# Optimization experiments

Hardware: AMD Instinct MI355X
Metric: run time of the kernel (lower is better)

The kernel has to match this reference:

```python
import jax, jax.numpy as jnp
import numpy as np

B, H, S, DK = 2, 16, 2048, 64


def setup_inputs() -> dict:
    key = jax.random.key(0)
    k1, k2, k3, k4 = jax.random.split(key, 4)
    Q = jax.random.normal(k1, (B, H, S, DK), dtype=jnp.float32)
    K = jax.random.normal(k2, (B, H, S, DK), dtype=jnp.float32)
    V = jax.random.normal(k3, (B, H, S, DK), dtype=jnp.float32)
    attn_mask = jax.random.randint(k4, (B, 1, S, S), 0, 2).astype(jnp.bool_)
    return {"Q": Q, "K": K, "V": V, "attn_mask": attn_mask}


def reference(Q, K, V, attn_mask):
    d_k = Q.shape[-1]
    scale = 1.0 / jnp.sqrt(jnp.asarray(d_k, dtype=Q.dtype))
    # scores: [B,H,S,S]
    scores = jnp.einsum('bhqd,bhkd->bhqk', Q, K) * scale
    scores = jnp.where(attn_mask, jnp.asarray(-1e9, dtype=scores.dtype), scores)
    attn = jax.nn.softmax(scores, axis=-1)
    # dropout in eval mode (identity) for deterministic reference
    return jnp.einsum('bhqk,bhkd->bhqd', attn, V)
```

## Files before the change

kernel.cpp:

```cpp
#include <hip/hip_runtime.h>
#include <hip/hip_bf16.h>

#define Bdim 2
#define Hdim 16
#define Sdim 2048
#define Ddim 64
#define KVBLK 64
#define NT (Sdim / KVBLK)
#define WQ 32
#define NWAVE 4
#define QTILE (WQ * NWAVE)
#define QSCL (0.125f * 1.44269504088896f)
#define SCALE 0.125f
#define BUFE 8192
#define VOFF 4096

typedef __bf16 bf16x8 __attribute__((ext_vector_type(8)));
typedef float  f32x4  __attribute__((ext_vector_type(4)));
typedef float  f32x16 __attribute__((ext_vector_type(16)));
typedef unsigned u32x4 __attribute__((ext_vector_type(4)));

__device__ __forceinline__ void gll16(const __bf16* g, __bf16* l) {
  __builtin_amdgcn_global_load_lds(
      (const __attribute__((address_space(1))) void*)g,
      (__attribute__((address_space(3))) void*)l, 16, 0, 0);
}
__device__ __forceinline__ unsigned cvtpk_raw(float lo, float hi) {
  unsigned r;
  asm("v_cvt_pk_bf16_f32 %0, %1, %2" : "=v"(r) : "v"(lo), "v"(hi));
  return r;
}
template <bool SW>
__device__ __forceinline__ unsigned pko(float a, float b) {
  return SW ? cvtpk_raw(b, a) : cvtpk_raw(a, b);
}
__device__ __forceinline__ unsigned cvtpk(float a, float b, bool sw) {
  const float lo = sw ? b : a;
  const float hi = sw ? a : b;
  return cvtpk_raw(lo, hi);
}
template <bool SW>
__device__ __forceinline__ void packAll(const float (&sv0)[16],
                                        const float (&sv1)[16],
                                        unsigned (&pw)[16]) {
#pragma unroll
  for (int ks = 0; ks < 4; ++ks) {
    const int rb = 8 * (ks & 1);
    if (ks < 2) {
      pw[ks * 4 + 0] = pko<SW>(sv0[rb + 0], sv0[rb + 1]);
      pw[ks * 4 + 1] = pko<SW>(sv0[rb + 2], sv0[rb + 3]);
      pw[ks * 4 + 2] = pko<SW>(sv0[rb + 4], sv0[rb + 5]);
      pw[ks * 4 + 3] = pko<SW>(sv0[rb + 6], sv0[rb + 7]);
    } else {
      pw[ks * 4 + 0] = pko<SW>(sv1[rb + 0], sv1[rb + 1]);
      pw[ks * 4 + 1] = pko<SW>(sv1[rb + 2], sv1[rb + 3]);
      pw[ks * 4 + 2] = pko<SW>(sv1[rb + 4], sv1[rb + 5]);
      pw[ks * 4 + 3] = pko<SW>(sv1[rb + 6], sv1[rb + 7]);
    }
  }
}

__global__ __launch_bounds__(256) void prep_all(
    const void* __restrict__ mask, unsigned long long* __restrict__ packed,
    const float* __restrict__ K, const float* __restrict__ V,
    __bf16* __restrict__ Kb, __bf16* __restrict__ Vt) {
  __shared__ __bf16 tile[64][72];
  const int t = threadIdx.x;

  if (blockIdx.x < 512) {
    const int nwords = Bdim * Sdim * (Sdim / 64);
    const unsigned* m32 = (const unsigned*)mask;
    const unsigned char* m8 = (const unsigned char*)mask;
    int gid = blockIdx.x * 256 + t;
    int lane = gid & 63;
    int wid = gid >> 6;
    const int nwaves = 512 * 256 / 64;
    bool isBytes = __any(m32[lane] > 1u);
    for (int w = wid; w < nwords; w += nwaves) {
      int v = isBytes ? (int)m8[(size_t)w * 64 + lane]
                      : (int)m32[(size_t)w * 64 + lane];
      unsigned long long bal = __ballot(v != 0);
      if (lane == 0) packed[w] = bal;
    }
    return;
  }

  const int idx = blockIdx.x - 512;
  const int bh = idx >> 5, st = idx & 31;
  const int r = t >> 2, c0 = (t & 3) << 4;
  {
    const float* ks = K + ((size_t)bh * Sdim + st * 64 + r) * Ddim + c0;
    bf16x8 o0, o1;
#pragma unroll
    for (int j = 0; j < 8; ++j) o0[j] = (__bf16)ks[j];
#pragma unroll
    for (int j = 0; j < 8; ++j) o1[j] = (__bf16)ks[8 + j];
    __bf16* kd = Kb + ((size_t)bh * Sdim + st * 64 + r) * Ddim + c0;
    *(bf16x8*)kd = o0;
    *(bf16x8*)(kd + 8) = o1;
  }
  {
    const float* vs = V + ((size_t)bh * Sdim + st * 64 + r) * Ddim + c0;
#pragma unroll
    for (int j = 0; j < 16; ++j) tile[r][c0 + j] = (__bf16)vs[j];
  }
  __syncthreads();
  {
    const int d = t >> 2, s0 = (t & 3) << 4;
    __bf16 o[16];
#pragma unroll
    for (int j = 0; j < 16; ++j) o[j] = tile[s0 + j][d];
    __bf16* dst = Vt + ((size_t)bh * Ddim + d) * Sdim + st * 64 + s0;
    *(bf16x8*)dst = *(bf16x8*)&o[0];
    *(bf16x8*)(dst + 8) = *(bf16x8*)&o[8];
  }
}

__global__ __launch_bounds__(256, 2) void attn4(
    const float* __restrict__ Q, const __bf16* __restrict__ Kb,
    const __bf16* __restrict__ Vt,
    const unsigned long long* __restrict__ maskP, float* __restrict__ Out) {
  __shared__ alignas(16) __bf16 sm[3 * BUFE];

  const int tid = threadIdx.x;
  const int lane = tid & 63;
  const int w = tid >> 6;
  const int l31 = lane & 31;
  const int hi = lane >> 5;
  const int rsw = l31 & 7;

  const int bid = blockIdx.x;
  const int bh = bid & 31;
  const int qt = bid >> 5;
  const int b = bh >> 4;
  const int qrow = qt * QTILE + w * WQ + l31;

  const __bf16* Kbase = Kb + (size_t)bh * Sdim * Ddim;
  const __bf16* Vbase = Vt + (size_t)bh * (size_t)Ddim * Sdim;
  const unsigned long long* mp =
      maskP + ((size_t)b * Sdim + qrow) * (Sdim / 64);

  const bool sw = (cvtpk_raw(0.0f, 1.0f) & 0xFFFFu) != 0u;

  bf16x8 qf[4];
  {
    const float* qs = Q + ((size_t)bh * Sdim + qrow) * Ddim;
#pragma unroll
    for (int step = 0; step < 4; ++step) {
      const int d0 = step * 16 + hi * 8;
      float4 a = *(const float4*)(qs + d0);
      float4 c = *(const float4*)(qs + d0 + 4);
      u32x4 f;
      f[0] = cvtpk(a.x * QSCL, a.y * QSCL, sw);
      f[1] = cvtpk(a.z * QSCL, a.w * QSCL, sw);
      f[2] = cvtpk(c.x * QSCL, c.y * QSCL, sw);
      f[3] = cvtpk(c.z * QSCL, c.w * QSCL, sw);
      qf[step] = __builtin_bit_cast(bf16x8, f);
    }
  }

  const int srow = 16 * w + (lane >> 3);
  const int sblk = (lane & 7) ^ ((lane >> 3) & 7);
  const int dstw = w * 1024;

#define STAGE(off_, kt_)                                                        \
  do {                                                                          \
    const __bf16* kp_ = Kbase + ((size_t)(kt_)*KVBLK + srow) * Ddim + sblk * 8; \
    gll16(kp_, &sm[(off_) + dstw]);                                             \
    gll16(kp_ + 8 * Ddim, &sm[(off_) + dstw + 512]);                            \
    const __bf16* vp_ =                                                         \
        Vbase + (size_t)srow * Sdim + (size_t)(kt_)*KVBLK + sblk * 8;           \
    gll16(vp_, &sm[(off_) + VOFF + dstw]);                                      \
    gll16(vp_ + 8 * Sdim, &sm[(off_) + VOFF + dstw + 512]);                     \
  } while (0)

  f32x16 otA = {0,0,0,0,0,0,0,0,0,0,0,0,0,0,0,0};
  f32x16 otB = {0,0,0,0,0,0,0,0,0,0,0,0,0,0,0,0};
  float lrow = 0.f;

  unsigned long long mwCur = mp[0];
  STAGE(0, 0);
  int rdOff = 0, stOff = BUFE;

#pragma unroll 1
  for (int kt = 0; kt < NT; ++kt) {
    const unsigned long long mwNext = mp[kt + 1 < NT ? kt + 1 : NT - 1];
    if (kt + 1 < NT) {
      STAGE(stOff, kt + 1);
      asm volatile("s_waitcnt vmcnt(5)" ::: "memory");
    } else {
      asm volatile("s_waitcnt vmcnt(1)" ::: "memory");
    }
    __builtin_amdgcn_s_barrier();
    __builtin_amdgcn_sched_barrier(0);

    f32x16 st0 = {0,0,0,0,0,0,0,0,0,0,0,0,0,0,0,0};
    f32x16 st1 = {0,0,0,0,0,0,0,0,0,0,0,0,0,0,0,0};
    __builtin_amdgcn_s_setprio(1);
#pragma unroll
    for (int step = 0; step < 4; ++step) {
      bf16x8 kf = *(const bf16x8*)&sm[rdOff + l31 * 64 + (((step * 2 + hi) ^ rsw) << 3)];
      st0 = __builtin_amdgcn_mfma_f32_32x32x16_bf16(kf, qf[step], st0, 0, 0, 0);
    }
#pragma unroll
    for (int step = 0; step < 4; ++step) {
      bf16x8 kf = *(const bf16x8*)&sm[rdOff + (32 + l31) * 64 + (((step * 2 + hi) ^ rsw) << 3)];
      st1 = __builtin_amdgcn_mfma_f32_32x32x16_bf16(kf, qf[step], st1, 0, 0, 0);
    }
    __builtin_amdgcn_s_setprio(0);

    float sv0[16], sv1[16];
    const unsigned w0s = ((unsigned)mwCur) >> (hi * 4);
    const unsigned w1s = ((unsigned)(mwCur >> 32)) >> (hi * 4);
#pragma unroll
    for (int r = 0; r < 16; ++r) {
      const int cr = (r & 3) + 8 * (r >> 2);
      const float e0 = __builtin_amdgcn_exp2f(st0[r]);
      const float e1 = __builtin_amdgcn_exp2f(st1[r]);
      sv0[r] = ((w0s >> cr) & 1u) ? 0.f : e0;
      sv1[r] = ((w1s >> cr) & 1u) ? 0.f : e1;
    }

    float s8[8];
#pragma unroll
    for (int j = 0; j < 8; ++j)
      s8[j] = (sv0[j] + sv0[j + 8]) + (sv1[j] + sv1[j + 8]);
    lrow += ((s8[0] + s8[4]) + (s8[1] + s8[5])) +
            ((s8[2] + s8[6]) + (s8[3] + s8[7]));

    unsigned pw[16];
    if (!sw) packAll<false>(sv0, sv1, pw);
    else     packAll<true>(sv0, sv1, pw);
    bf16x8 pb[4];
#pragma unroll
    for (int ks = 0; ks < 4; ++ks) {
      const unsigned W0 = pw[ks * 4 + 0], W1 = pw[ks * 4 + 1];
      const unsigned X0 = pw[ks * 4 + 2], X1 = pw[ks * 4 + 3];
      const unsigned s1 = hi ? W0 : X0;
      const unsigned s2 = hi ? W1 : X1;
      const unsigned r1 = __shfl_xor(s1, 32, 64);
      const unsigned r2 = __shfl_xor(s2, 32, 64);
      u32x4 wv;
      wv[0] = hi ? r1 : W0;
      wv[1] = hi ? r2 : W1;
      wv[2] = hi ? X0 : r1;
      wv[3] = hi ? X1 : r2;
      pb[ks] = __builtin_bit_cast(bf16x8, wv);
    }

    __builtin_amdgcn_s_setprio(1);
#pragma unroll
    for (int ks = 0; ks < 4; ++ks) {
      bf16x8 vf = *(const bf16x8*)&sm[rdOff + VOFF + l31 * 64 + (((ks * 2 + hi) ^ rsw) << 3)];
      otA = __builtin_amdgcn_mfma_f32_32x32x16_bf16(vf, pb[ks], otA, 0, 0, 0);
    }
#pragma unroll
    for (int ks = 0; ks < 4; ++ks) {
      bf16x8 vf = *(const bf16x8*)&sm[rdOff + VOFF + (32 + l31) * 64 + (((ks * 2 + hi) ^ rsw) << 3)];
      otB = __builtin_amdgcn_mfma_f32_32x32x16_bf16(vf, pb[ks], otB, 0, 0, 0);
    }
    __builtin_amdgcn_s_setprio(0);

    mwCur = mwNext;
    rdOff = stOff;
    stOff = (stOff == 2 * BUFE) ? 0 : stOff + BUFE;
  }
#undef STAGE

  lrow += __shfl_xor(lrow, 32, 64);
  const float inv = 1.f / (lrow + 1e-30f);
  float* orow = Out + ((size_t)bh * Sdim + qrow) * Ddim;
#pragma unroll
  for (int g = 0; g < 4; ++g) {
    const int d0 = 8 * g + 4 * hi;
    float4 va = {otA[4 * g] * inv, otA[4 * g + 1] * inv,
                 otA[4 * g + 2] * inv, otA[4 * g + 3] * inv};
    float4 vb = {otB[4 * g] * inv, otB[4 * g + 1] * inv,
                 otB[4 * g + 2] * inv, otB[4 * g + 3] * inv};
    *(float4*)(orow + d0) = va;
    *(float4*)(orow + 32 + d0) = vb;
  }
}

__global__ __launch_bounds__(256) void attn_fallback(
    const float* __restrict__ Q, const float* __restrict__ K,
    const float* __restrict__ V, const void* __restrict__ maskRaw,
    float* __restrict__ Out) {
  __shared__ alignas(16) __bf16 Kl[KVBLK * Ddim];
  __shared__ alignas(16) __bf16 Vts[Ddim * KVBLK];
  __shared__ alignas(16) __bf16 Pl[4][16 * 64];

  const int tid = threadIdx.x;
  const int lane = tid & 63;
  const int w = tid >> 6;
  const int lhi = lane >> 4;
  const int llo = lane & 15;

  const int qt = blockIdx.x;
  const int bh = blockIdx.y;
  const int b = bh >> 4;
  const int qbase = qt * 64;

  const float* Qp = Q + (size_t)bh * Sdim * Ddim;
  const float* Kp = K + (size_t)bh * Sdim * Ddim;
  const float* Vp = V + (size_t)bh * Sdim * Ddim;

  bool maskBytes = __any(((const unsigned*)maskRaw)[lane] > 1u);

  bf16x8 qf0, qf1;
  {
    const int qr = qbase + w * 16 + llo;
    const float* src = Qp + (size_t)qr * Ddim + lhi * 8;
#pragma unroll
    for (int i = 0; i < 8; ++i) qf0[i] = (__bf16)(src[i] * SCALE);
#pragma unroll
    for (int i = 0; i < 8; ++i) qf1[i] = (__bf16)(src[32 + i] * SCALE);
  }

  f32x4 acc[4] = {{0.f,0.f,0.f,0.f},{0.f,0.f,0.f,0.f},
                  {0.f,0.f,0.f,0.f},{0.f,0.f,0.f,0.f}};
  float mrow[4], lrw[4];
#pragma unroll
  for (int r = 0; r < 4; ++r) { mrow[r] = -3.0e38f; lrw[r] = 0.f; }

  for (int kt = 0; kt < NT; ++kt) {
    __syncthreads();
    {
      int r = tid >> 2;
      int c0 = (tid & 3) << 4;
      const float* ks = Kp + (size_t)(kt * KVBLK + r) * Ddim + c0;
      const float* vs = Vp + (size_t)(kt * KVBLK + r) * Ddim + c0;
      float kv[16], vv[16];
#pragma unroll
      for (int j = 0; j < 4; ++j) {
        *(float4*)(&kv[j * 4]) = *(const float4*)(ks + j * 4);
        *(float4*)(&vv[j * 4]) = *(const float4*)(vs + j * 4);
      }
      const int swzK = (r & 7) << 3;
      bf16x8 k0v, k1v;
#pragma unroll
      for (int j = 0; j < 8; ++j) { k0v[j] = (__bf16)kv[j]; k1v[j] = (__bf16)kv[8 + j]; }
      *(bf16x8*)&Kl[r * 64 + (c0 ^ swzK)] = k0v;
      *(bf16x8*)&Kl[r * 64 + ((c0 + 8) ^ swzK)] = k1v;
#pragma unroll
      for (int j = 0; j < 16; ++j) {
        int d = c0 + j;
        Vts[d * 64 + (r ^ ((d & 7) << 3))] = (__bf16)vv[j];
      }
    }
    __syncthreads();

    float sv[4][4];
#pragma unroll
    for (int cb = 0; cb < 4; ++cb) {
      int krow = cb * 16 + llo;
      int swz = (krow & 7) << 3;
      bf16x8 kf0 = *(const bf16x8*)&Kl[krow * 64 + ((lhi * 8) ^ swz)];
      bf16x8 kf1 = *(const bf16x8*)&Kl[krow * 64 + ((32 + lhi * 8) ^ swz)];
      f32x4 s = {0.f, 0.f, 0.f, 0.f};
      s = __builtin_amdgcn_mfma_f32_16x16x32_bf16(qf0, kf0, s, 0, 0, 0);
      s = __builtin_amdgcn_mfma_f32_16x16x32_bf16(qf1, kf1, s, 0, 0, 0);
#pragma unroll
      for (int r = 0; r < 4; ++r) {
        size_t q = qbase + w * 16 + lhi * 4 + r;
        size_t k = (size_t)kt * KVBLK + cb * 16 + llo;
        size_t idx = ((size_t)b * Sdim + q) * Sdim + k;
        bool masked = maskBytes ? (((const unsigned char*)maskRaw)[idx] != 0)
                                : (((const int*)maskRaw)[idx] != 0);
        sv[cb][r] = masked ? -1e9f : s[r];
      }
    }

    float corr[4], tsum[4];
#pragma unroll
    for (int r = 0; r < 4; ++r) {
      float mx = fmaxf(fmaxf(sv[0][r], sv[1][r]), fmaxf(sv[2][r], sv[3][r]));
#pragma unroll
      for (int off = 1; off < 16; off <<= 1)
        mx = fmaxf(mx, __shfl_xor(mx, off, 64));
      float mnew = fmaxf(mrow[r], mx);
      corr[r] = __expf(mrow[r] - mnew);
      mrow[r] = mnew;
      tsum[r] = 0.f;
    }
#pragma unroll
    for (int cb = 0; cb < 4; ++cb) {
#pragma unroll
      for (int r = 0; r < 4; ++r) {
        float p = __expf(sv[cb][r] - mrow[r]);
        tsum[r] += p;
        int row = lhi * 4 + r;
        int col = cb * 16 + llo;
        Pl[w][row * 64 + (col ^ ((row & 7) << 3))] = (__bf16)p;
      }
    }
#pragma unroll
    for (int r = 0; r < 4; ++r) {
      float s = tsum[r];
#pragma unroll
      for (int off = 1; off < 16; off <<= 1)
        s += __shfl_xor(s, off, 64);
      lrw[r] = lrw[r] * corr[r] + s;
#pragma unroll
      for (int db = 0; db < 4; ++db) acc[db][r] *= corr[r];
    }
    asm volatile("s_waitcnt lgkmcnt(0)" ::: "memory");

    bf16x8 pf0 = *(const bf16x8*)&Pl[w][llo * 64 + ((lhi * 8) ^ ((llo & 7) << 3))];
    bf16x8 pf1 = *(const bf16x8*)&Pl[w][llo * 64 + ((32 + lhi * 8) ^ ((llo & 7) << 3))];
#pragma unroll
    for (int db = 0; db < 4; ++db) {
      int d = db * 16 + llo;
      int swz = (d & 7) << 3;
      bf16x8 vf0 = *(const bf16x8*)&Vts[d * 64 + ((lhi * 8) ^ swz)];
      bf16x8 vf1 = *(const bf16x8*)&Vts[d * 64 + ((32 + lhi * 8) ^ swz)];
      acc[db] = __builtin_amdgcn_mfma_f32_16x16x32_bf16(pf0, vf0, acc[db], 0, 0, 0);
      acc[db] = __builtin_amdgcn_mfma_f32_16x16x32_bf16(pf1, vf1, acc[db], 0, 0, 0);
    }
  }

#pragma unroll
  for (int r = 0; r < 4; ++r) {
    float inv = 1.f / lrw[r];
    int q = qbase + w * 16 + lhi * 4 + r;
    float* dst = Out + ((size_t)bh * Sdim + q) * Ddim + llo;
#pragma unroll
    for (int db = 0; db < 4; ++db) dst[db * 16] = acc[db][r] * inv;
  }
}

extern "C" void kernel_launch(void* const* d_in, const int* in_sizes, int n_in,
                              void* d_out, int out_size, void* d_ws, size_t ws_size,
                              hipStream_t stream) {
  const float* Q = (const float*)d_in[0];
  const float* K = (const float*)d_in[1];
  const float* V = (const float*)d_in[2];
  const void* mask = d_in[3];
  float* out = (float*)d_out;

  const size_t packed_bytes =
      (size_t)Bdim * Sdim * (Sdim / 64) * sizeof(unsigned long long);
  const size_t tensor_bf16 = (size_t)Bdim * Hdim * Sdim * Ddim * 2;

  if (ws_size >= packed_bytes + 2 * tensor_bf16) {
    unsigned long long* packed = (unsigned long long*)d_ws;
    __bf16* Kb = (__bf16*)((char*)d_ws + packed_bytes);
    __bf16* Vt = (__bf16*)((char*)d_ws + packed_bytes + tensor_bf16);
    prep_all<<<512 + Bdim * Hdim * (Sdim / 64), 256, 0, stream>>>(
        mask, packed, K, V, Kb, Vt);
    attn4<<<(Sdim / QTILE) * Bdim * Hdim, 256, 0, stream>>>(Q, Kb, Vt, packed, out);
  } else {
    attn_fallback<<<dim3(Sdim / 64, Bdim * Hdim), 256, 0, stream>>>(Q, K, V, mask, out);
  }
}
```

Baseline: 101.0 us.

## Load K and V tiles directly from global into registers, dropping LDS staging

Removes the triple-buffered LDS staging via global_load_lds and the per-iteration workgroup barrier. Each wave now loads its K and V fragments straight from global memory into registers, with K for the next tile prefetched during the softmax. This removes barrier sync and LDS traffic, but the four waves of a block now each fetch the same K/V data separately, so L2/global traffic rises and V-load latency is less hidden.

```diff
diff --git a/kernel.cpp b/kernel.cpp
--- a/kernel.cpp
+++ b/kernel.cpp
@@ -12,19 +12,12 @@
 #define QTILE (WQ * NWAVE)
 #define QSCL (0.125f * 1.44269504088896f)
 #define SCALE 0.125f
-#define BUFE 8192
-#define VOFF 4096
 
 typedef __bf16 bf16x8 __attribute__((ext_vector_type(8)));
 typedef float  f32x4  __attribute__((ext_vector_type(4)));
 typedef float  f32x16 __attribute__((ext_vector_type(16)));
 typedef unsigned u32x4 __attribute__((ext_vector_type(4)));
 
-__device__ __forceinline__ void gll16(const __bf16* g, __bf16* l) {
-  __builtin_amdgcn_global_load_lds(
-      (const __attribute__((address_space(1))) void*)g,
-      (__attribute__((address_space(3))) void*)l, 16, 0, 0);
-}
 __device__ __forceinline__ unsigned cvtpk_raw(float lo, float hi) {
   unsigned r;
   asm("v_cvt_pk_bf16_f32 %0, %1, %2" : "=v"(r) : "v"(lo), "v"(hi));
@@ -116,18 +109,15 @@
   }
 }
 
-__global__ __launch_bounds__(256, 2) void attn4(
+__global__ __launch_bounds__(256, 2) void attn6(
     const float* __restrict__ Q, const __bf16* __restrict__ Kb,
     const __bf16* __restrict__ Vt,
     const unsigned long long* __restrict__ maskP, float* __restrict__ Out) {
-  __shared__ alignas(16) __bf16 sm[3 * BUFE];
-
   const int tid = threadIdx.x;
   const int lane = tid & 63;
   const int w = tid >> 6;
   const int l31 = lane & 31;
   const int hi = lane >> 5;
-  const int rsw = l31 & 7;
 
   const int bid = blockIdx.x;
   const int bh = bid & 31;
@@ -159,55 +149,52 @@
     }
   }
 
-  const int srow = 16 * w + (lane >> 3);
-  const int sblk = (lane & 7) ^ ((lane >> 3) & 7);
-  const int dstw = w * 1024;
-
-#define STAGE(off_, kt_)                                                        \
-  do {                                                                          \
-    const __bf16* kp_ = Kbase + ((size_t)(kt_)*KVBLK + srow) * Ddim + sblk * 8; \
-    gll16(kp_, &sm[(off_) + dstw]);                                             \
-    gll16(kp_ + 8 * Ddim, &sm[(off_) + dstw + 512]);                            \
-    const __bf16* vp_ =                                                         \
-        Vbase + (size_t)srow * Sdim + (size_t)(kt_)*KVBLK + sblk * 8;           \
-    gll16(vp_, &sm[(off_) + VOFF + dstw]);                                      \
-    gll16(vp_ + 8 * Sdim, &sm[(off_) + VOFF + dstw + 512]);                     \
-  } while (0)
+  const __bf16* kp0 = Kbase + (size_t)l31 * Ddim + hi * 8;
+  const __bf16* vp0 = Vbase + (size_t)l31 * Sdim + hi * 8;
 
   f32x16 otA = {0,0,0,0,0,0,0,0,0,0,0,0,0,0,0,0};
   f32x16 otB = {0,0,0,0,0,0,0,0,0,0,0,0,0,0,0,0};
   float lrow = 0.f;
 
+  bf16x8 ka[8];
+#pragma unroll
+  for (int s = 0; s < 4; ++s) {
+    ka[s] = *(const bf16x8*)(kp0 + s * 16);
+    ka[s + 4] = *(const bf16x8*)(kp0 + 32 * Ddim + s * 16);
+  }
   unsigned long long mwCur = mp[0];
-  STAGE(0, 0);
-  int rdOff = 0, stOff = BUFE;
 
 #pragma unroll 1
   for (int kt = 0; kt < NT; ++kt) {
-    const unsigned long long mwNext = mp[kt + 1 < NT ? kt + 1 : NT - 1];
-    if (kt + 1 < NT) {
-      STAGE(stOff, kt + 1);
-      asm volatile("s_waitcnt vmcnt(5)" ::: "memory");
-    } else {
-      asm volatile("s_waitcnt vmcnt(1)" ::: "memory");
-    }
-    __builtin_amdgcn_s_barrier();
-    __builtin_amdgcn_sched_barrier(0);
+    const __bf16* vp = vp0 + (size_t)kt * KVBLK;
+    bf16x8 vv[8];
+#pragma unroll
+    for (int s = 0; s < 4; ++s) {
+      vv[s] = *(const bf16x8*)(vp + s * 16);
+      vv[s + 4] = *(const bf16x8*)(vp + 32 * Sdim + s * 16);
+    }
+    const int ktn = (kt + 1 < NT) ? kt + 1 : 0;
+    const unsigned long long mwNext = mp[ktn];
 
     f32x16 st0 = {0,0,0,0,0,0,0,0,0,0,0,0,0,0,0,0};
     f32x16 st1 = {0,0,0,0,0,0,0,0,0,0,0,0,0,0,0,0};
     __builtin_amdgcn_s_setprio(1);
 #pragma unroll
-    for (int step = 0; step < 4; ++step) {
-      bf16x8 kf = *(const bf16x8*)&sm[rdOff + l31 * 64 + (((step * 2 + hi) ^ rsw) << 3)];
-      st0 = __builtin_amdgcn_mfma_f32_32x32x16_bf16(kf, qf[step], st0, 0, 0, 0);
-    }
-#pragma unroll
-    for (int step = 0; step < 4; ++step) {
-      bf16x8 kf = *(const bf16x8*)&sm[rdOff + (32 + l31) * 64 + (((step * 2 + hi) ^ rsw) << 3)];
-      st1 = __builtin_amdgcn_mfma_f32_32x32x16_bf16(kf, qf[step], st1, 0, 0, 0);
-    }
+    for (int step = 0; step < 4; ++step)
+      st0 = __builtin_amdgcn_mfma_f32_32x32x16_bf16(ka[step], qf[step], st0, 0, 0, 0);
+#pragma unroll
+    for (int step = 0; step < 4; ++step)
+      st1 = __builtin_amdgcn_mfma_f32_32x32x16_bf16(ka[step + 4], qf[step], st1, 0, 0, 0);
     __builtin_amdgcn_s_setprio(0);
+
+    {
+      const __bf16* kp = kp0 + (size_t)ktn * KVBLK * Ddim;
+#pragma unroll
+      for (int s = 0; s < 4; ++s) {
+        ka[s] = *(const bf16x8*)(kp + s * 16);
+        ka[s + 4] = *(const bf16x8*)(kp + 32 * Ddim + s * 16);
+      }
+    }
 
     float sv0[16], sv1[16];
     const unsigned w0s = ((unsigned)mwCur) >> (hi * 4);
@@ -250,22 +237,15 @@
 
     __builtin_amdgcn_s_setprio(1);
 #pragma unroll
-    for (int ks = 0; ks < 4; ++ks) {
-      bf16x8 vf = *(const bf16x8*)&sm[rdOff + VOFF + l31 * 64 + (((ks * 2 + hi) ^ rsw) << 3)];
-      otA = __builtin_amdgcn_mfma_f32_32x32x16_bf16(vf, pb[ks], otA, 0, 0, 0);
-    }
-#pragma unroll
-    for (int ks = 0; ks < 4; ++ks) {
-      bf16x8 vf = *(const bf16x8*)&sm[rdOff + VOFF + (32 + l31) * 64 + (((ks * 2 + hi) ^ rsw) << 3)];
-      otB = __builtin_amdgcn_mfma_f32_32x32x16_bf16(vf, pb[ks], otB, 0, 0, 0);
-    }
+    for (int ks = 0; ks < 4; ++ks)
+      otA = __builtin_amdgcn_mfma_f32_32x32x16_bf16(vv[ks], pb[ks], otA, 0, 0, 0);
+#pragma unroll
+    for (int ks = 0; ks < 4; ++ks)
+      otB = __builtin_amdgcn_mfma_f32_32x32x16_bf16(vv[ks + 4], pb[ks], otB, 0, 0, 0);
     __builtin_amdgcn_s_setprio(0);
 
     mwCur = mwNext;
-    rdOff = stOff;
-    stOff = (stOff == 2 * BUFE) ? 0 : stOff + BUFE;
-  }
-#undef STAGE
+  }
 
   lrow += __shfl_xor(lrow, 32, 64);
   const float inv = 1.f / (lrow + 1e-30f);
@@ -448,7 +428,7 @@
     __bf16* Vt = (__bf16*)((char*)d_ws + packed_bytes + tensor_bf16);
     prep_all<<<512 + Bdim * Hdim * (Sdim / 64), 256, 0, stream>>>(
         mask, packed, K, V, Kb, Vt);
-    attn4<<<(Sdim / QTILE) * Bdim * Hdim, 256, 0, stream>>>(Q, Kb, Vt, packed, out);
+    attn6<<<(Sdim / QTILE) * Bdim * Hdim, 256, 0, stream>>>(Q, Kb, Vt, packed, out);
   } else {
     attn_fallback<<<dim3(Sdim / 64, Bdim * Hdim), 256, 0, stream>>>(Q, K, V, mask, out);
   }
```

After: 168.8 us. 1.67x slower.
